# Optimization experiments

Hardware: AMD Instinct MI355X
Metric: run time of the kernel (lower is better)

## Reference

```python
import jax, jax.numpy as jnp
import numpy as np

B, F, T, D, O = 8192, 512, 64, 6, 128
N_INTERNAL = 2 ** D - 1  # 63
N_LEAVES = 2 ** D        # 64


def smooth_step(t):
    tc = jnp.clip(t, -0.5, 0.5)
    return -2.0 * tc ** 3 + 1.5 * tc + 0.5


def setup_inputs() -> dict:
    key = jax.random.key(0)
    k1, k2, k3, k4 = jax.random.split(key, 4)
    x = jax.random.normal(k1, (B, F), dtype=jnp.float32)
    # Stacked per-node Linear weights in BFS (heap) order: node i -> row i.
    W_nodes = jax.random.normal(k2, (N_INTERNAL, F, T), dtype=jnp.float32) * (1.0 / np.sqrt(F))
    b_nodes = jax.random.normal(k3, (N_INTERNAL, T), dtype=jnp.float32) * 0.01
    # Per-leaf mixing weight [out_features, num_trees], leaves in BFS order.
    W_leaf = jax.random.normal(k4, (N_LEAVES, O, T), dtype=jnp.float32)
    return {"x": x, "W_nodes": W_nodes, "b_nodes": b_nodes, "W_leaf": W_leaf}


def reference(x, W_nodes, b_nodes, W_leaf):
    n_internal = W_nodes.shape[0]
    depth = int(np.log2(n_internal + 1))
    # All internal-node gates in one stacked GEMM: [B, n_internal, T]
    s = smooth_step(jnp.einsum('bf,nft->bnt', x, W_nodes) + b_nodes[None, :, :])
    b, _, t = s.shape
    prob = jnp.ones((b, 1, t), dtype=s.dtype)  # root prob
    start = 0
    for lvl in range(depth):
        width = 2 ** lvl
        s_l = s[:, start:start + width]  # [B, width, T], nodes at this level
        start += width
        # node local j -> children local 2j (left, prob*s) and 2j+1 (right, prob*(1-s))
        prob = jnp.stack([prob * s_l, prob * (1.0 - s_l)], axis=2).reshape(b, 2 * width, t)
    # prob: [B, n_leaves, T]; mix per-leaf, per-tree weights -> [B, O]
    out = jnp.einsum('blt,lot->bo', prob, W_leaf)
    return out
```

## Files before the change

### kernel.cpp

```cpp
#include <hip/hip_runtime.h>
#include <hip/hip_fp16.h>

#define BATCH 8192
#define FDIM  512
#define NTREE 64
#define NODES 63
#define ODIM  128
#define NJP   4096
#define K2    4096
#define TPG   8

typedef _Float16 f16;
typedef _Float16 f16x2 __attribute__((ext_vector_type(2)));
typedef _Float16 f16x8 __attribute__((ext_vector_type(8)));
typedef float    f32x4 __attribute__((ext_vector_type(4)));

#define XH_OFF   0
#define XH_SZ    ((size_t)BATCH*FDIM*2)
#define WNH_OFF  (XH_OFF + XH_SZ)
#define WNH_SZ   ((size_t)NJP*FDIM*2)
#define WLT_OFF  (WNH_OFF + WNH_SZ)
#define WLT_SZ   ((size_t)ODIM*K2*2)
#define PS_OFF   (WLT_OFF + WLT_SZ)
#define PS_SZ    ((size_t)TPG*BATCH*ODIM*4)
#define WS_NEEDED (PS_OFF + PS_SZ)

__device__ __forceinline__ float smooth_step_f(float t) {
    float tc = fminf(fmaxf(t, -0.5f), 0.5f);
    return fmaf(tc, fmaf(-2.0f * tc, tc, 1.5f), 0.5f);
}

__device__ __forceinline__ void async16(const void* g, void* l) {
    __builtin_amdgcn_global_load_lds((__attribute__((address_space(1))) void*)g,
                                     (__attribute__((address_space(3))) void*)l,
                                     16, 0, 0);
}

__device__ __forceinline__ int sw_off(int row, int g) {
    return ((row >> 3) * 512) + (((row & 7) * 8 + (g ^ (row & 7))) * 8);
}

#define XBLK 4096
#define WLBLK 128
__global__ __launch_bounds__(256)
void prep_kernel(const float* __restrict__ x, const float* __restrict__ wn,
                 const float* __restrict__ wl,
                 f16* __restrict__ xh, f16* __restrict__ wnh, f16* __restrict__ wlt)
{
    __shared__ __align__(16) char smem[16640];
    const int bid = blockIdx.x;

    if (bid < XBLK) {
        size_t i = ((size_t)bid * 256 + threadIdx.x) * 4;
        float4 v = *(const float4*)(x + i);
        f16* o = xh + i;
        o[0] = (f16)v.x; o[1] = (f16)v.y; o[2] = (f16)v.z; o[3] = (f16)v.w;
        return;
    }
    if (bid < XBLK + WLBLK) {
        f16 (*tile)[72] = (f16(*)[72])smem;
        const int o    = bid - XBLK;
        const int lane = threadIdx.x & 63;
        const int w    = threadIdx.x >> 6;
        #pragma unroll
        for (int lc = 0; lc < 16; ++lc) {
            int l = w * 16 + lc;
            tile[lane][l] = (f16)wl[(size_t)l * (ODIM * NTREE) + o * 64 + lane];
        }
        __syncthreads();
        f16* orow = wlt + (size_t)o * K2;
        #pragma unroll
        for (int c = 0; c < 2; ++c) {
            int idx = (threadIdx.x * 2 + c) * 8;
            int t = idx >> 6, l = idx & 63;
            f16x8 v;
            #pragma unroll
            for (int e = 0; e < 8; ++e) v[e] = tile[t][l + e];
            *(f16x8*)(orow + idx) = v;
        }
        return;
    }
    {
        const int id   = bid - (XBLK + WLBLK);
        const int n    = id & 63;
        const int f0   = (id >> 6) * 64;
        const int lane = threadIdx.x & 63;
        const int w    = threadIdx.x >> 6;
        if (n == NODES) {
            #pragma unroll
            for (int tc = 0; tc < 16; ++tc) {
                int t = w * 16 + tc;
                wnh[(size_t)(t * 64 + NODES) * FDIM + f0 + lane] = (f16)0.0f;
            }
            return;
        }
        float (*tile)[65] = (float(*)[65])smem;
        const float* src = wn + (size_t)n * (FDIM * NTREE);
        #pragma unroll
        for (int i = 0; i < 16; ++i) {
            int fl = w * 16 + i;
            tile[fl][lane] = src[(size_t)(f0 + fl) * NTREE + lane];
        }
        __syncthreads();
        #pragma unroll
        for (int i = 0; i < 16; ++i) {
            int t = w * 16 + i;
            wnh[(size_t)(t * 64 + n) * FDIM + f0 + lane] = (f16)tile[lane][t];
        }
    }
}

__global__ __launch_bounds__(256, 2)
void fused_tree(const f16* __restrict__ xh, const f16* __restrict__ wnh,
                const float* __restrict__ bn, const f16* __restrict__ wlt,
                float* __restrict__ partial)
{
    __shared__ f16 SH[33024];
    f16* CT = SH + 16384;
    const int tid  = threadIdx.x;
    const int lane = tid & 63;
    const int w    = tid >> 6;
    const int wm   = w & 1;
    const int wn   = w >> 1;
    const int row0 = blockIdx.x * 128;
    const int tpg  = blockIdx.y;

    const int lr = lane >> 3;
    const int lg = (lane & 7) ^ lr;
    const int frow = tid & 127;
    const int ftr  = tid >> 7;

    f32x4 lacc[4][4] = {};

    for (int tpi = 0; tpi < 4; ++tpi) {
        const int tp = tpg * 4 + tpi;
        const int j0 = tp * 128;

        f32x4 acc[4][4] = {};
        for (int k0 = 0; k0 < FDIM; k0 += 64) {
            #pragma unroll
            for (int q = 0; q < 8; ++q) {
                int id = w * 8 + q;
                if (id < 16) {
                    int r = id * 8 + lr;
                    async16(xh + (size_t)(row0 + r) * FDIM + k0 + lg * 8, &SH[id * 512 + lane * 8]);
                } else {
                    int c = id - 16;
                    int r = c * 8 + lr;
                    async16(wnh + (size_t)(j0 + r) * FDIM + k0 + lg * 8, &SH[8192 + c * 512 + lane * 8]);
                }
            }
            __syncthreads();
            #pragma unroll
            for (int ks = 0; ks < 2; ++ks) {
                int g = ks * 4 + (lane >> 4);
                f16x8 bfr[4];
                #pragma unroll
                for (int tn = 0; tn < 4; ++tn) {
                    int j = wn * 64 + tn * 16 + (lane & 15);
                    bfr[tn] = *(const f16x8*)&SH[8192 + sw_off(j, g)];
                }
                #pragma unroll
                for (int tm = 0; tm < 4; ++tm) {
                    int m = wm * 64 + tm * 16 + (lane & 15);
                    f16x8 afr = *(const f16x8*)&SH[sw_off(m, g)];
                    #pragma unroll
                    for (int tn = 0; tn < 4; ++tn)
                        acc[tm][tn] = __builtin_amdgcn_mfma_f32_16x16x32_f16(afr, bfr[tn], acc[tm][tn], 0, 0, 0);
                }
            }
            __syncthreads();
        }

        #pragma unroll
        for (int q = 0; q < 8; ++q) {
            int id = w * 8 + q;
            int h = id >> 4, c = id & 15;
            int o = c * 8 + lr;
            async16(wlt + (size_t)o * K2 + j0 + h * 64 + lg * 8,
                    &SH[h * 8192 + c * 512 + lane * 8]);
        }

        #pragma unroll
        for (int tn = 0; tn < 4; ++tn) {
            int col = wn * 64 + tn * 16 + (lane & 15);
            int nn  = col & 63;
            int tt  = (j0 + col) >> 6;
            float bias = (nn < NODES) ? bn[nn * NTREE + tt] : 0.0f;
            #pragma unroll
            for (int tm = 0; tm < 4; ++tm) {
                #pragma unroll
                for (int r = 0; r < 4; ++r) {
                    int row = wm * 64 + tm * 16 + (lane >> 4) * 4 + r;
                    CT[row * 130 + col] = (f16)smooth_step_f(acc[tm][tn][r] + bias);
                }
            }
        }
        __syncthreads();

        f16x8 ov[8];
        {
            const f16* gp = &CT[frow * 130 + ftr * 64];
            float g[64];
            #pragma unroll
            for (int c = 0; c < 32; ++c) {
                f16x2 v = *(const f16x2*)(gp + 2 * c);
                g[2 * c]     = (float)v[0];
                g[2 * c + 1] = (float)v[1];
            }
            float pr[32];
            pr[0] = 1.0f;
            int bse = 0;
            #pragma unroll
            for (int lvl = 0; lvl < 5; ++lvl) {
                const int width = 1 << lvl;
                #pragma unroll
                for (int i = width - 1; i >= 0; --i) {
                    float p = pr[i], s = g[bse + i];
                    pr[2 * i]     = p * s;
                    pr[2 * i + 1] = p * (1.0f - s);
                }
                bse += width;
            }
            #pragma unroll
            for (int i = 0; i < 32; ++i) {
                float s5 = g[31 + i];
                float p  = pr[i];
                ov[i >> 2][(i & 3) * 2]     = (f16)(p * s5);
                ov[i >> 2][(i & 3) * 2 + 1] = (f16)(p * (1.0f - s5));
            }
        }
        __syncthreads();

        #pragma unroll
        for (int g2 = 0; g2 < 8; ++g2)
            *(f16x8*)&SH[16384 + ftr * 8192 + sw_off(frow, g2)] = ov[g2];
        __syncthreads();

        #pragma unroll
        for (int ks2 = 0; ks2 < 4; ++ks2) {
            int h  = ks2 >> 1;
            int gg = (ks2 & 1) * 4 + (lane >> 4);
            f16x8 bfr[4];
            #pragma unroll
            for (int tn = 0; tn < 4; ++tn) {
                int o = wn * 64 + tn * 16 + (lane & 15);
                bfr[tn] = *(const f16x8*)&SH[h * 8192 + sw_off(o, gg)];
            }
            #pragma unroll
            for (int tm = 0; tm < 4; ++tm) {
                int m = wm * 64 + tm * 16 + (lane & 15);
                f16x8 afr = *(const f16x8*)&SH[16384 + h * 8192 + sw_off(m, gg)];
                #pragma unroll
                for (int tn = 0; tn < 4; ++tn)
                    lacc[tm][tn] = __builtin_amdgcn_mfma_f32_16x16x32_f16(afr, bfr[tn], lacc[tm][tn], 0, 0, 0);
            }
        }
        __syncthreads();
    }

    float* dst = partial + (size_t)tpg * BATCH * ODIM;
    #pragma unroll
    for (int tn = 0; tn < 4; ++tn) {
        int o = wn * 64 + tn * 16 + (lane & 15);
        #pragma unroll
        for (int tm = 0; tm < 4; ++tm) {
            #pragma unroll
            for (int r = 0; r < 4; ++r) {
                int row = row0 + wm * 64 + tm * 16 + (lane >> 4) * 4 + r;
                dst[(size_t)row * ODIM + o] = lacc[tm][tn][r];
            }
        }
    }
}

__global__ void reduce_kernel(const float* __restrict__ partial, float* __restrict__ out) {
    size_t i = ((size_t)blockIdx.x * blockDim.x + threadIdx.x) * 4;
    f32x4 a = *(const f32x4*)(partial + i);
    #pragma unroll
    for (int k = 1; k < TPG; ++k)
        a += *(const f32x4*)(partial + (size_t)k * BATCH * ODIM + i);
    *(f32x4*)(out + i) = a;
}

#define ROWS 8
__global__ __launch_bounds__(256, 2)
void soft_tree_fallback(const float* __restrict__ x, const float* __restrict__ Wn,
                        const float* __restrict__ bn, const float* __restrict__ Wl,
                        float* __restrict__ out)
{
    __shared__ __half s_lds[ROWS][NODES][NTREE];
    const int lane = threadIdx.x & 63;
    const int w    = threadIdx.x >> 6;
    const long row0 = (long)blockIdx.x * ROWS;
    for (int n = w; n < NODES; n += 4) {
        const float* wp = Wn + ((long)n * FDIM) * NTREE + lane;
        const float* xp = x + row0 * FDIM;
        float acc[ROWS];
        #pragma unroll
        for (int r = 0; r < ROWS; ++r) acc[r] = 0.0f;
        #pragma unroll 8
        for (int f = 0; f < FDIM; ++f) {
            float wv = wp[(long)f * NTREE];
            #pragma unroll
            for (int r = 0; r < ROWS; ++r)
                acc[r] = fmaf(xp[r * FDIM + f], wv, acc[r]);
        }
        float bias = bn[n * NTREE + lane];
        #pragma unroll
        for (int r = 0; r < ROWS; ++r)
            s_lds[r][n][lane] = __float2half(smooth_step_f(acc[r] + bias));
    }
    __syncthreads();
    const int r0 = w * 2, r1 = w * 2 + 1;
    float pr0[64], pr1[64];
    {
        pr0[0] = 1.0f; pr1[0] = 1.0f;
        int base = 0;
        #pragma unroll
        for (int lvl = 0; lvl < 6; ++lvl) {
            const int width = 1 << lvl;
            #pragma unroll
            for (int i = width - 1; i >= 0; --i) {
                float sa = __half2float(s_lds[r0][base + i][lane]);
                float sb = __half2float(s_lds[r1][base + i][lane]);
                float pa = pr0[i], pb = pr1[i];
                pr0[2 * i] = pa * sa; pr0[2 * i + 1] = pa * (1.0f - sa);
                pr1[2 * i] = pb * sb; pr1[2 * i + 1] = pb * (1.0f - sb);
            }
            base += width;
        }
    }
    for (int o = 0; o < ODIM; ++o) {
        const float* wlp = Wl + (long)o * NTREE + lane;
        float c0 = 0.0f, c1 = 0.0f;
        #pragma unroll
        for (int l = 0; l < 64; ++l) {
            float wv = wlp[(long)l * (ODIM * NTREE)];
            c0 = fmaf(pr0[l], wv, c0);
            c1 = fmaf(pr1[l], wv, c1);
        }
        #pragma unroll
        for (int off = 32; off > 0; off >>= 1) {
            c0 += __shfl_xor(c0, off, 64);
            c1 += __shfl_xor(c1, off, 64);
        }
        if (lane == 0) {
            out[(row0 + r0) * ODIM + o] = c0;
            out[(row0 + r1) * ODIM + o] = c1;
        }
    }
}

extern "C" void kernel_launch(void* const* d_in, const int* in_sizes, int n_in,
                              void* d_out, int out_size, void* d_ws, size_t ws_size,
                              hipStream_t stream) {
    const float* x  = (const float*)d_in[0];
    const float* Wn = (const float*)d_in[1];
    const float* bn = (const float*)d_in[2];
    const float* Wl = (const float*)d_in[3];
    float* out = (float*)d_out;

    if (ws_size < WS_NEEDED) {
        soft_tree_fallback<<<BATCH / ROWS, 256, 0, stream>>>(x, Wn, bn, Wl, out);
        return;
    }

    f16*   xh  = (f16*)((char*)d_ws + XH_OFF);
    f16*   wnh = (f16*)((char*)d_ws + WNH_OFF);
    f16*   wlt = (f16*)((char*)d_ws + WLT_OFF);
    float* ps  = (float*)((char*)d_ws + PS_OFF);

    prep_kernel<<<XBLK + WLBLK + 512, 256, 0, stream>>>(x, Wn, Wl, xh, wnh, wlt);
    fused_tree<<<dim3(BATCH / 128, TPG), 256, 0, stream>>>(xh, wnh, bn, wlt, ps);
    reduce_kernel<<<(BATCH * ODIM) / (256 * 4), 256, 0, stream>>>(ps, out);
}
```

Measured before the change: 157.4 us.

## Fuse split-K reduction into tree kernel via last-block counter; widen K tile

Removes the separate reduce kernel. Each fused_tree block bumps a per-row-tile atomic counter, and the last of the TPG blocks sums the partials for its rows into the output. Counters are reset in the prep kernel. The first GEMM's K step also doubles to 128, halving the number of syncs per K loop, and the LDS regions are reassigned so the gate tile and leaf weights no longer overlap the larger staging buffers. This saves a kernel launch and some partial-buffer traffic, at the cost of atomics, threadfences and a serialized tail reduction in the last-arriving blocks.

```diff
diff --git a/kernel.cpp b/kernel.cpp
--- a/kernel.cpp
+++ b/kernel.cpp
@@ -23,7 +23,9 @@
 #define WLT_SZ   ((size_t)ODIM*K2*2)
 #define PS_OFF   (WLT_OFF + WLT_SZ)
 #define PS_SZ    ((size_t)TPG*BATCH*ODIM*4)
-#define WS_NEEDED (PS_OFF + PS_SZ)
+#define CNT_OFF  (PS_OFF + PS_SZ)
+#define CNT_SZ   (64 * sizeof(int))
+#define WS_NEEDED (CNT_OFF + CNT_SZ)
 
 __device__ __forceinline__ float smooth_step_f(float t) {
     float tc = fminf(fmaxf(t, -0.5f), 0.5f);
@@ -45,12 +47,14 @@
 __global__ __launch_bounds__(256)
 void prep_kernel(const float* __restrict__ x, const float* __restrict__ wn,
                  const float* __restrict__ wl,
-                 f16* __restrict__ xh, f16* __restrict__ wnh, f16* __restrict__ wlt)
+                 f16* __restrict__ xh, f16* __restrict__ wnh, f16* __restrict__ wlt,
+                 int* __restrict__ cnt)
 {
     __shared__ __align__(16) char smem[16640];
     const int bid = blockIdx.x;
 
     if (bid < XBLK) {
+        if (bid == 0 && threadIdx.x < 64) cnt[threadIdx.x] = 0;
         size_t i = ((size_t)bid * 256 + threadIdx.x) * 4;
         float4 v = *(const float4*)(x + i);
         f16* o = xh + i;
@@ -113,10 +117,11 @@
 __global__ __launch_bounds__(256, 2)
 void fused_tree(const f16* __restrict__ xh, const f16* __restrict__ wnh,
                 const float* __restrict__ bn, const f16* __restrict__ wlt,
-                float* __restrict__ partial)
+                float* __restrict__ partial, int* __restrict__ cnt,
+                float* __restrict__ outp)
 {
     __shared__ f16 SH[33024];
-    f16* CT = SH + 16384;
+    __shared__ int sflag;
     const int tid  = threadIdx.x;
     const int lane = tid & 63;
     const int w    = tid >> 6;
@@ -137,33 +142,34 @@
         const int j0 = tp * 128;
 
         f32x4 acc[4][4] = {};
-        for (int k0 = 0; k0 < FDIM; k0 += 64) {
-            #pragma unroll
-            for (int q = 0; q < 8; ++q) {
-                int id = w * 8 + q;
-                if (id < 16) {
-                    int r = id * 8 + lr;
-                    async16(xh + (size_t)(row0 + r) * FDIM + k0 + lg * 8, &SH[id * 512 + lane * 8]);
-                } else {
-                    int c = id - 16;
-                    int r = c * 8 + lr;
-                    async16(wnh + (size_t)(j0 + r) * FDIM + k0 + lg * 8, &SH[8192 + c * 512 + lane * 8]);
-                }
+        for (int k0 = 0; k0 < FDIM; k0 += 128) {
+            #pragma unroll
+            for (int q = 0; q < 16; ++q) {
+                int id  = w * 16 + q;
+                int isB = id >> 5;
+                int e   = id & 31;
+                int h   = e >> 4, c = e & 15;
+                int r   = c * 8 + lr;
+                const f16* src = isB
+                    ? (wnh + (size_t)(j0 + r) * FDIM + k0 + h * 64 + lg * 8)
+                    : (xh  + (size_t)(row0 + r) * FDIM + k0 + h * 64 + lg * 8);
+                async16(src, &SH[isB * 16384 + h * 8192 + c * 512 + lane * 8]);
             }
             __syncthreads();
             #pragma unroll
-            for (int ks = 0; ks < 2; ++ks) {
-                int g = ks * 4 + (lane >> 4);
+            for (int hk = 0; hk < 4; ++hk) {
+                int h = hk >> 1;
+                int g = (hk & 1) * 4 + (lane >> 4);
                 f16x8 bfr[4];
                 #pragma unroll
                 for (int tn = 0; tn < 4; ++tn) {
                     int j = wn * 64 + tn * 16 + (lane & 15);
-                    bfr[tn] = *(const f16x8*)&SH[8192 + sw_off(j, g)];
+                    bfr[tn] = *(const f16x8*)&SH[16384 + h * 8192 + sw_off(j, g)];
                 }
                 #pragma unroll
                 for (int tm = 0; tm < 4; ++tm) {
                     int m = wm * 64 + tm * 16 + (lane & 15);
-                    f16x8 afr = *(const f16x8*)&SH[sw_off(m, g)];
+                    f16x8 afr = *(const f16x8*)&SH[h * 8192 + sw_off(m, g)];
                     #pragma unroll
                     for (int tn = 0; tn < 4; ++tn)
                         acc[tm][tn] = __builtin_amdgcn_mfma_f32_16x16x32_f16(afr, bfr[tn], acc[tm][tn], 0, 0, 0);
@@ -178,7 +184,7 @@
             int h = id >> 4, c = id & 15;
             int o = c * 8 + lr;
             async16(wlt + (size_t)o * K2 + j0 + h * 64 + lg * 8,
-                    &SH[h * 8192 + c * 512 + lane * 8]);
+                    &SH[16640 + h * 8192 + c * 512 + lane * 8]);
         }
 
         #pragma unroll
@@ -192,7 +198,7 @@
                 #pragma unroll
                 for (int r = 0; r < 4; ++r) {
                     int row = wm * 64 + tm * 16 + (lane >> 4) * 4 + r;
-                    CT[row * 130 + col] = (f16)smooth_step_f(acc[tm][tn][r] + bias);
+                    SH[row * 130 + col] = (f16)smooth_step_f(acc[tm][tn][r] + bias);
                 }
             }
         }
@@ -200,7 +206,7 @@
 
         f16x8 ov[8];
         {
-            const f16* gp = &CT[frow * 130 + ftr * 64];
+            const f16* gp = &SH[frow * 130 + ftr * 64];
             float g[64];
             #pragma unroll
             for (int c = 0; c < 32; ++c) {
@@ -234,7 +240,7 @@
 
         #pragma unroll
         for (int g2 = 0; g2 < 8; ++g2)
-            *(f16x8*)&SH[16384 + ftr * 8192 + sw_off(frow, g2)] = ov[g2];
+            *(f16x8*)&SH[ftr * 8192 + sw_off(frow, g2)] = ov[g2];
         __syncthreads();
 
         #pragma unroll
@@ -245,12 +251,12 @@
             #pragma unroll
             for (int tn = 0; tn < 4; ++tn) {
                 int o = wn * 64 + tn * 16 + (lane & 15);
-                bfr[tn] = *(const f16x8*)&SH[h * 8192 + sw_off(o, gg)];
+                bfr[tn] = *(const f16x8*)&SH[16640 + h * 8192 + sw_off(o, gg)];
             }
             #pragma unroll
             for (int tm = 0; tm < 4; ++tm) {
                 int m = wm * 64 + tm * 16 + (lane & 15);
-                f16x8 afr = *(const f16x8*)&SH[16384 + h * 8192 + sw_off(m, gg)];
+                f16x8 afr = *(const f16x8*)&SH[h * 8192 + sw_off(m, gg)];
                 #pragma unroll
                 for (int tn = 0; tn < 4; ++tn)
                     lacc[tm][tn] = __builtin_amdgcn_mfma_f32_16x16x32_f16(afr, bfr[tn], lacc[tm][tn], 0, 0, 0);
@@ -272,15 +278,24 @@
             }
         }
     }
-}
-
-__global__ void reduce_kernel(const float* __restrict__ partial, float* __restrict__ out) {
-    size_t i = ((size_t)blockIdx.x * blockDim.x + threadIdx.x) * 4;
-    f32x4 a = *(const f32x4*)(partial + i);
-    #pragma unroll
-    for (int k = 1; k < TPG; ++k)
-        a += *(const f32x4*)(partial + (size_t)k * BATCH * ODIM + i);
-    *(f32x4*)(out + i) = a;
+
+    __threadfence();
+    if (tid == 0) sflag = atomicAdd(&cnt[blockIdx.x], 1);
+    __syncthreads();
+    if (sflag == TPG - 1) {
+        __threadfence();
+        #pragma unroll
+        for (int it = 0; it < 16; ++it) {
+            int idx = it * 256 + tid;
+            int row = idx >> 5, c4 = idx & 31;
+            size_t off = (size_t)(row0 + row) * ODIM + c4 * 4;
+            f32x4 a = *(const f32x4*)(partial + off);
+            #pragma unroll
+            for (int k = 1; k < TPG; ++k)
+                a += *(const f32x4*)(partial + (size_t)k * BATCH * ODIM + off);
+            *(f32x4*)(outp + off) = a;
+        }
+    }
 }
 
 #define ROWS 8
@@ -370,8 +385,8 @@
     f16*   wnh = (f16*)((char*)d_ws + WNH_OFF);
     f16*   wlt = (f16*)((char*)d_ws + WLT_OFF);
     float* ps  = (float*)((char*)d_ws + PS_OFF);
-
-    prep_kernel<<<XBLK + WLBLK + 512, 256, 0, stream>>>(x, Wn, Wl, xh, wnh, wlt);
-    fused_tree<<<dim3(BATCH / 128, TPG), 256, 0, stream>>>(xh, wnh, bn, wlt, ps);
-    reduce_kernel<<<(BATCH * ODIM) / (256 * 4), 256, 0, stream>>>(ps, out);
-}
+    int*   cnt = (int*)((char*)d_ws + CNT_OFF);
+
+    prep_kernel<<<XBLK + WLBLK + 512, 256, 0, stream>>>(x, Wn, Wl, xh, wnh, wlt, cnt);
+    fused_tree<<<dim3(BATCH / 128, TPG), 256, 0, stream>>>(xh, wnh, bn, wlt, ps, cnt, out);
+}
```

Result: slower. 256.3 us (+62.8%).

## Halve fused_tree shared memory by staging leaf GEMM in two passes

Applied to the files above, without the earlier changes.

The fused kernel's shared buffer is cut from about 66KB to about 33KB. The CT gate tile now reuses the start of SH, and the leaf-mixing GEMM runs in two half-K passes that each stage one half of the probabilities and W_leaf. This is meant to let more blocks fit on each CU and raise occupancy. In exchange, the W_leaf async load no longer overlaps the smooth-step and tree-probability compute, and each tile adds extra barriers. The prep kernel also writes x in fp16 with one vectorized 8-byte store instead of four scalar stores.

```diff
diff --git a/kernel.cpp b/kernel.cpp
--- a/kernel.cpp
+++ b/kernel.cpp
@@ -12,6 +12,7 @@
 
 typedef _Float16 f16;
 typedef _Float16 f16x2 __attribute__((ext_vector_type(2)));
+typedef _Float16 f16x4 __attribute__((ext_vector_type(4)));
 typedef _Float16 f16x8 __attribute__((ext_vector_type(8)));
 typedef float    f32x4 __attribute__((ext_vector_type(4)));
 
@@ -53,8 +54,8 @@
     if (bid < XBLK) {
         size_t i = ((size_t)bid * 256 + threadIdx.x) * 4;
         float4 v = *(const float4*)(x + i);
-        f16* o = xh + i;
-        o[0] = (f16)v.x; o[1] = (f16)v.y; o[2] = (f16)v.z; o[3] = (f16)v.w;
+        f16x4 o4 = { (f16)v.x, (f16)v.y, (f16)v.z, (f16)v.w };
+        *(f16x4*)(xh + i) = o4;
         return;
     }
     if (bid < XBLK + WLBLK) {
@@ -115,8 +116,7 @@
                 const float* __restrict__ bn, const f16* __restrict__ wlt,
                 float* __restrict__ partial)
 {
-    __shared__ f16 SH[33024];
-    f16* CT = SH + 16384;
+    __shared__ f16 SH[16640];
     const int tid  = threadIdx.x;
     const int lane = tid & 63;
     const int w    = tid >> 6;
@@ -173,15 +173,6 @@
         }
 
         #pragma unroll
-        for (int q = 0; q < 8; ++q) {
-            int id = w * 8 + q;
-            int h = id >> 4, c = id & 15;
-            int o = c * 8 + lr;
-            async16(wlt + (size_t)o * K2 + j0 + h * 64 + lg * 8,
-                    &SH[h * 8192 + c * 512 + lane * 8]);
-        }
-
-        #pragma unroll
         for (int tn = 0; tn < 4; ++tn) {
             int col = wn * 64 + tn * 16 + (lane & 15);
             int nn  = col & 63;
@@ -192,7 +183,7 @@
                 #pragma unroll
                 for (int r = 0; r < 4; ++r) {
                     int row = wm * 64 + tm * 16 + (lane >> 4) * 4 + r;
-                    CT[row * 130 + col] = (f16)smooth_step_f(acc[tm][tn][r] + bias);
+                    SH[row * 130 + col] = (f16)smooth_step_f(acc[tm][tn][r] + bias);
                 }
             }
         }
@@ -200,7 +191,7 @@
 
         f16x8 ov[8];
         {
-            const f16* gp = &CT[frow * 130 + ftr * 64];
+            const f16* gp = &SH[frow * 130 + ftr * 64];
             float g[64];
             #pragma unroll
             for (int c = 0; c < 32; ++c) {
@@ -233,30 +224,41 @@
         __syncthreads();
 
         #pragma unroll
-        for (int g2 = 0; g2 < 8; ++g2)
-            *(f16x8*)&SH[16384 + ftr * 8192 + sw_off(frow, g2)] = ov[g2];
-        __syncthreads();
-
-        #pragma unroll
-        for (int ks2 = 0; ks2 < 4; ++ks2) {
-            int h  = ks2 >> 1;
-            int gg = (ks2 & 1) * 4 + (lane >> 4);
-            f16x8 bfr[4];
-            #pragma unroll
-            for (int tn = 0; tn < 4; ++tn) {
-                int o = wn * 64 + tn * 16 + (lane & 15);
-                bfr[tn] = *(const f16x8*)&SH[h * 8192 + sw_off(o, gg)];
-            }
-            #pragma unroll
-            for (int tm = 0; tm < 4; ++tm) {
-                int m = wm * 64 + tm * 16 + (lane & 15);
-                f16x8 afr = *(const f16x8*)&SH[16384 + h * 8192 + sw_off(m, gg)];
-                #pragma unroll
-                for (int tn = 0; tn < 4; ++tn)
-                    lacc[tm][tn] = __builtin_amdgcn_mfma_f32_16x16x32_f16(afr, bfr[tn], lacc[tm][tn], 0, 0, 0);
-            }
-        }
-        __syncthreads();
+        for (int h = 0; h < 2; ++h) {
+            if (ftr == h) {
+                #pragma unroll
+                for (int g2 = 0; g2 < 8; ++g2)
+                    *(f16x8*)&SH[sw_off(frow, g2)] = ov[g2];
+            }
+            #pragma unroll
+            for (int q = 0; q < 4; ++q) {
+                int c = w * 4 + q;
+                int o = c * 8 + lr;
+                async16(wlt + (size_t)o * K2 + j0 + h * 64 + lg * 8,
+                        &SH[8192 + c * 512 + lane * 8]);
+            }
+            __syncthreads();
+
+            #pragma unroll
+            for (int ks = 0; ks < 2; ++ks) {
+                int g = ks * 4 + (lane >> 4);
+                f16x8 bfr[4];
+                #pragma unroll
+                for (int tn = 0; tn < 4; ++tn) {
+                    int o = wn * 64 + tn * 16 + (lane & 15);
+                    bfr[tn] = *(const f16x8*)&SH[8192 + sw_off(o, g)];
+                }
+                #pragma unroll
+                for (int tm = 0; tm < 4; ++tm) {
+                    int m = wm * 64 + tm * 16 + (lane & 15);
+                    f16x8 afr = *(const f16x8*)&SH[sw_off(m, g)];
+                    #pragma unroll
+                    for (int tn = 0; tn < 4; ++tn)
+                        lacc[tm][tn] = __builtin_amdgcn_mfma_f32_16x16x32_f16(afr, bfr[tn], lacc[tm][tn], 0, 0, 0);
+                }
+            }
+            __syncthreads();
+        }
     }
 
     float* dst = partial + (size_t)tpg * BATCH * ODIM;
```

After: 149.2 us. -5.2%, faster.
